# Kernel optimization log

Hardware: AMD Instinct MI355X
Metric: run time of the kernel (lower is better)

Reference implementation:

```python
import jax, jax.numpy as jnp
import numpy as np

N = 4096
IN_F = 256
H = 4
D = 64
WIN = 128
HALF = WIN // 2
TAU = 0.5
TOP_K = 32


def setup_inputs() -> dict:
    key = jax.random.key(0)
    ks = jax.random.split(key, 5)
    node_features = jax.random.normal(ks[0], (N, IN_F), dtype=jnp.float32)
    s = 1.0 / np.sqrt(IN_F)
    Wq = jax.random.normal(ks[1], (IN_F, H * D), dtype=jnp.float32) * s
    bq = jax.random.normal(ks[2], (H * D,), dtype=jnp.float32) * 0.01
    Wk = jax.random.normal(ks[3], (IN_F, H * D), dtype=jnp.float32) * s
    bk = jax.random.normal(ks[4], (H * D,), dtype=jnp.float32) * 0.01
    num_nodes_per_graph = jnp.full((8,), 512, dtype=jnp.int32)  # 8 graphs x 512 = N
    return {"node_features": node_features, "Wq": Wq, "bq": bq, "Wk": Wk,
            "bk": bk, "num_nodes_per_graph": num_nodes_per_graph, "num_relation": 1}


def reference(node_features, Wq, bq, Wk, bk, num_nodes_per_graph, num_relation):
    n = node_features.shape[0]
    scale = jnp.sqrt(jnp.asarray(D, node_features.dtype))

    Q = (node_features @ Wq + bq).reshape(n, H, D)
    K = (node_features @ Wk + bk).reshape(n, H, D)

    # segment boundaries (graph.num_nodes.repeat(num_relation) -> cumsum -> searchsorted)
    segment = jnp.tile(num_nodes_per_graph, num_relation)
    cum = jnp.cumsum(segment)
    i = jnp.arange(n)
    pos = jnp.searchsorted(cum, i, side='right')
    seg_start = jnp.where(pos == 0, 0, cum[jnp.maximum(pos - 1, 0)])
    seg_end = cum[jnp.minimum(pos, cum.shape[0] - 1)]

    start = jnp.maximum(seg_start, i - HALF)  # [N]
    end = jnp.minimum(seg_end, i + HALF)      # [N]

    gather_idx = start[:, None] + jnp.arange(WIN)[None, :]
    valid = gather_idx < end[:, None]
    gi = jnp.clip(gather_idx, 0, n - 1)
    Kw = jnp.where(valid[:, :, None, None], K[gi], 0.0)

    # scores over full window incl. zero padding (faithful: original does not mask softmax)
    scores = jnp.einsum('nhd,nmhd->nhm', Q, Kw) / scale / TAU
    attn = jax.nn.softmax(scores, axis=-1).mean(axis=1)

    # scatter attention rows into dense N x N (padded slots add 0)
    output = jnp.zeros((n, n), node_features.dtype).at[i[:, None], gi].add(
        jnp.where(valid, attn, 0.0))

    # gumbel_softmax_top_k(output, tau, hard=self.k) -> hard=True (k truthy)
    g = jax.random.gumbel(jax.random.key(42), output.shape, output.dtype)
    y_soft = jax.nn.softmax((output + g) / TAU, axis=-1)
    topk_idx = jax.lax.top_k(output, TOP_K)[1]                  # [N, TOP_K]
    y_hard = jnp.zeros_like(output).at[i[:, None], topk_idx].set(1.0)
    y = jax.lax.stop_gradient(y_hard - y_soft) + y_soft
    return y
```

## Files before the change

kernel.cpp:

```cpp
#include <hip/hip_runtime.h>

#define NF   256
#define HD   256
#define NH   4
#define DH   64
#define WINS 128
#define HALFW 64
#define TOPK 32
#define GR   8

__global__ __launch_bounds__(256) void qk_gemm_kernel(
    const float* __restrict__ X,
    const float* __restrict__ Wq, const float* __restrict__ bq,
    const float* __restrict__ Wk, const float* __restrict__ bk,
    float* __restrict__ Qb, float* __restrict__ Kt, int n)
{
    const bool isK = (blockIdx.y != 0);
    const float* W   = isK ? Wk : Wq;
    const float* bia = isK ? bk : bq;

    __shared__ float feat[GR][NF];
    const int rowBase = blockIdx.x * GR;
    const int t = threadIdx.x;

    {
        const float4* src = (const float4*)(X + (size_t)rowBase * NF);
        float4* dst = (float4*)&feat[0][0];
        dst[t]       = src[t];
        dst[t + 256] = src[t + 256];
    }
    __syncthreads();

    float acc[GR];
#pragma unroll
    for (int r = 0; r < GR; ++r) acc[r] = 0.f;

#pragma unroll 4
    for (int k = 0; k < NF; k += 4) {
        float w0 = W[(size_t)(k + 0) * HD + t];
        float w1 = W[(size_t)(k + 1) * HD + t];
        float w2 = W[(size_t)(k + 2) * HD + t];
        float w3 = W[(size_t)(k + 3) * HD + t];
#pragma unroll
        for (int r = 0; r < GR; ++r) {
            float4 f = *(const float4*)&feat[r][k];
            acc[r] += f.x * w0 + f.y * w1 + f.z * w2 + f.w * w3;
        }
    }
    float bias = bia[t];

    if (!isK) {
#pragma unroll
        for (int r = 0; r < GR; ++r)
            Qb[(size_t)(rowBase + r) * HD + t] = acc[r] + bias;
    } else {
        float4* o = (float4*)(Kt + (size_t)t * n + rowBase);
        o[0] = make_float4(acc[0] + bias, acc[1] + bias, acc[2] + bias, acc[3] + bias);
        o[1] = make_float4(acc[4] + bias, acc[5] + bias, acc[6] + bias, acc[7] + bias);
    }
}

__global__ __launch_bounds__(256) void attn_topk_kernel(
    const float* __restrict__ Q,
    const float* __restrict__ KT,
    const int* __restrict__ nnpg, int n_graphs,
    const int* __restrict__ nrel,
    float* __restrict__ out, int n)
{
    const int i    = blockIdx.x;
    const int t    = threadIdx.x;
    const int wave = t >> 6;
    const int lane = t & 63;

    __shared__ float qs[HD];
    __shared__ float pr[NH][WINS];
    __shared__ float attnv[WINS];
    __shared__ float slotval[WINS];

    int R = nrel[0];
    int total = n_graphs * R;
    int seg_start = 0, seg_end = n;
    int cum = 0;
    for (int e = 0; e < total; ++e) {
        int sz = nnpg[e % n_graphs];
        int nc = cum + sz;
        if (i < nc) { seg_start = cum; seg_end = nc; break; }
        cum = nc;
    }
    const int start = max(seg_start, i - HALFW);
    const int end   = min(seg_end,   i + HALFW);
    const int win   = end - start;

    qs[t] = Q[(size_t)i * HD + t];
    __syncthreads();

    const bool v0 = (lane      < win);
    const bool v1 = (lane + 64 < win);
    const int  j0 = v0 ? (start + lane)      : start;
    const int  j1 = v1 ? (start + lane + 64) : start;

    const float* kcol = KT + (size_t)(wave * DH) * n;
    const float* qh   = qs + wave * DH;

    float a0 = 0.f, a1 = 0.f;
#pragma unroll 8
    for (int d = 0; d < DH; ++d) {
        float qd = qh[d];
        const float* col = kcol + (size_t)d * n;
        a0 += qd * col[j0];
        a1 += qd * col[j1];
    }
    a0 = v0 ? a0 * 0.25f : 0.f;
    a1 = v1 ? a1 * 0.25f : 0.f;

    float mx = fmaxf(a0, a1);
#pragma unroll
    for (int off = 32; off > 0; off >>= 1) mx = fmaxf(mx, __shfl_xor(mx, off));
    float e0 = expf(a0 - mx), e1 = expf(a1 - mx);
    float sm = e0 + e1;
#pragma unroll
    for (int off = 32; off > 0; off >>= 1) sm += __shfl_xor(sm, off);
    pr[wave][lane]      = e0 / sm;
    pr[wave][lane + 64] = e1 / sm;
    __syncthreads();

    if (t < WINS) {
        float a = 0.25f * (pr[0][t] + pr[1][t] + pr[2][t] + pr[3][t]);
        attnv[t] = (t < win) ? a : -1.0f;
    }
    __syncthreads();

    if (t < WINS) {
        float v = attnv[t];
        int cnt = 0;
#pragma unroll
        for (int j4 = 0; j4 < WINS / 4; ++j4) {
            float4 a4 = *(const float4*)&attnv[j4 * 4];
            int jb = j4 * 4;
            cnt += (a4.x > v) || (a4.x == v && (jb + 0) < t);
            cnt += (a4.y > v) || (a4.y == v && (jb + 1) < t);
            cnt += (a4.z > v) || (a4.z == v && (jb + 2) < t);
            cnt += (a4.w > v) || (a4.w == v && (jb + 3) < t);
        }
        slotval[t] = (t < win && cnt < TOPK) ? 1.0f : 0.0f;
    }
    __syncthreads();

    float4* orow = (float4*)(out + (size_t)i * n);
    const int n4 = n >> 2;
    for (int c4 = t; c4 < n4; c4 += 256) {
        int c = c4 << 2;
        float4 v4 = make_float4(0.f, 0.f, 0.f, 0.f);
        if (c + 3 >= start && c < end) {
            int o = c - start;
            if (o     >= 0 && o     < WINS) v4.x = slotval[o];
            if (o + 1 >= 0 && o + 1 < WINS) v4.y = slotval[o + 1];
            if (o + 2 >= 0 && o + 2 < WINS) v4.z = slotval[o + 2];
            if (o + 3 >= 0 && o + 3 < WINS) v4.w = slotval[o + 3];
        }
        orow[c4] = v4;
    }
}

extern "C" void kernel_launch(void* const* d_in, const int* in_sizes, int n_in,
                              void* d_out, int out_size, void* d_ws, size_t ws_size,
                              hipStream_t stream)
{
    const float* X  = (const float*)d_in[0];
    const float* Wq = (const float*)d_in[1];
    const float* bq = (const float*)d_in[2];
    const float* Wk = (const float*)d_in[3];
    const float* bk = (const float*)d_in[4];
    const int* nnpg = (const int*)d_in[5];
    const int* nrel = (const int*)d_in[6];

    const int n = in_sizes[0] / NF;
    const int n_graphs = in_sizes[5];

    float* Qb = (float*)d_ws;
    float* Kt = Qb + (size_t)n * HD;
    float* out = (float*)d_out;

    dim3 gg(n / GR, 2);
    qk_gemm_kernel<<<gg, 256, 0, stream>>>(X, Wq, bq, Wk, bk, Qb, Kt, n);
    attn_topk_kernel<<<n, 256, 0, stream>>>(Qb, Kt, nnpg, n_graphs, nrel, out, n);
}
```

Measured before the change: 161.2 us.

## Map one wave per row in attention kernel, split zero fill, drop LDS staging

The attention kernel now gives each wave one output row and loops over the four heads itself. Q values are broadcast with readlane, and top-k ranking happens within the wave, so the block-level syncs and shared Q/probability buffers go away. The dense zero write of the output matrix moves to a separate grid-stride fill kernel, and the attention kernel scatters only the selected ones. The GEMM also stops staging X in LDS and reads it straight from global memory. The costs are an extra kernel launch, the full output written in a separate pass, and one wave now doing four heads of work serially.

```diff
diff --git a/kernel.cpp b/kernel.cpp
--- a/kernel.cpp
+++ b/kernel.cpp
@@ -8,6 +8,11 @@
 #define HALFW 64
 #define TOPK 32
 #define GR   8
+#define NPB  4
+
+__device__ __forceinline__ float readlane_f(float v, int l) {
+    return __uint_as_float(__builtin_amdgcn_readlane(__float_as_uint(v), l));
+}
 
 __global__ __launch_bounds__(256) void qk_gemm_kernel(
     const float* __restrict__ X,
@@ -19,17 +24,9 @@
     const float* W   = isK ? Wk : Wq;
     const float* bia = isK ? bk : bq;
 
-    __shared__ float feat[GR][NF];
+    const int t = threadIdx.x;
     const int rowBase = blockIdx.x * GR;
-    const int t = threadIdx.x;
-
-    {
-        const float4* src = (const float4*)(X + (size_t)rowBase * NF);
-        float4* dst = (float4*)&feat[0][0];
-        dst[t]       = src[t];
-        dst[t + 256] = src[t + 256];
-    }
-    __syncthreads();
+    const float* Xb = X + (size_t)rowBase * NF;
 
     float acc[GR];
 #pragma unroll
@@ -43,7 +40,7 @@
         float w3 = W[(size_t)(k + 3) * HD + t];
 #pragma unroll
         for (int r = 0; r < GR; ++r) {
-            float4 f = *(const float4*)&feat[r][k];
+            float4 f = *(const float4*)(Xb + r * NF + k);
             acc[r] += f.x * w0 + f.y * w1 + f.z * w2 + f.w * w3;
         }
     }
@@ -60,6 +57,14 @@
     }
 }
 
+__global__ __launch_bounds__(256) void fill_zero_kernel(float4* __restrict__ p, int n4)
+{
+    int idx = blockIdx.x * 256 + threadIdx.x;
+    int stride = gridDim.x * 256;
+    float4 z = make_float4(0.f, 0.f, 0.f, 0.f);
+    for (int c = idx; c < n4; c += stride) p[c] = z;
+}
+
 __global__ __launch_bounds__(256) void attn_topk_kernel(
     const float* __restrict__ Q,
     const float* __restrict__ KT,
@@ -67,15 +72,12 @@
     const int* __restrict__ nrel,
     float* __restrict__ out, int n)
 {
-    const int i    = blockIdx.x;
     const int t    = threadIdx.x;
     const int wave = t >> 6;
     const int lane = t & 63;
+    const int i    = blockIdx.x * NPB + wave;
 
-    __shared__ float qs[HD];
-    __shared__ float pr[NH][WINS];
-    __shared__ float attnv[WINS];
-    __shared__ float slotval[WINS];
+    __shared__ float attnv[NPB][WINS];
 
     int R = nrel[0];
     int total = n_graphs * R;
@@ -91,75 +93,69 @@
     const int end   = min(seg_end,   i + HALFW);
     const int win   = end - start;
 
-    qs[t] = Q[(size_t)i * HD + t];
-    __syncthreads();
+    const float* qrow = Q + (size_t)i * HD;
+    float qr[NH];
+#pragma unroll
+    for (int h = 0; h < NH; ++h) qr[h] = qrow[lane + h * DH];
 
     const bool v0 = (lane      < win);
     const bool v1 = (lane + 64 < win);
-    const int  j0 = v0 ? (start + lane)      : start;
-    const int  j1 = v1 ? (start + lane + 64) : start;
+    const int  j0 = start + min(lane,      win - 1);
+    const int  j1 = start + min(lane + 64, win - 1);
 
-    const float* kcol = KT + (size_t)(wave * DH) * n;
-    const float* qh   = qs + wave * DH;
+    float mean0 = 0.f, mean1 = 0.f;
+#pragma unroll
+    for (int h = 0; h < NH; ++h) {
+        const float* base = KT + (size_t)(h * DH) * n;
+        float a0 = 0.f, a1 = 0.f;
+#pragma unroll 8
+        for (int d = 0; d < DH; ++d) {
+            float qd = readlane_f(qr[h], d);
+            const float* col = base + (size_t)d * n;
+            a0 += qd * col[j0];
+            a1 += qd * col[j1];
+        }
+        a0 = v0 ? a0 * 0.25f : 0.f;
+        a1 = v1 ? a1 * 0.25f : 0.f;
 
-    float a0 = 0.f, a1 = 0.f;
-#pragma unroll 8
-    for (int d = 0; d < DH; ++d) {
-        float qd = qh[d];
-        const float* col = kcol + (size_t)d * n;
-        a0 += qd * col[j0];
-        a1 += qd * col[j1];
+        float mx = fmaxf(a0, a1);
+#pragma unroll
+        for (int off = 32; off > 0; off >>= 1) mx = fmaxf(mx, __shfl_xor(mx, off));
+        float e0 = expf(a0 - mx), e1 = expf(a1 - mx);
+        float sm = e0 + e1;
+#pragma unroll
+        for (int off = 32; off > 0; off >>= 1) sm += __shfl_xor(sm, off);
+        float inv = 1.f / sm;
+        mean0 += e0 * inv;
+        mean1 += e1 * inv;
     }
-    a0 = v0 ? a0 * 0.25f : 0.f;
-    a1 = v1 ? a1 * 0.25f : 0.f;
+    mean0 *= 0.25f;
+    mean1 *= 0.25f;
 
-    float mx = fmaxf(a0, a1);
+    attnv[wave][lane]      = v0 ? mean0 : -1.0f;
+    attnv[wave][lane + 64] = v1 ? mean1 : -1.0f;
+
+    float w0v = v0 ? mean0 : -1.0f;
+    float w1v = v1 ? mean1 : -1.0f;
+    int cnt0 = 0, cnt1 = 0;
+    const int s0 = lane, s1 = lane + 64;
 #pragma unroll
-    for (int off = 32; off > 0; off >>= 1) mx = fmaxf(mx, __shfl_xor(mx, off));
-    float e0 = expf(a0 - mx), e1 = expf(a1 - mx);
-    float sm = e0 + e1;
-#pragma unroll
-    for (int off = 32; off > 0; off >>= 1) sm += __shfl_xor(sm, off);
-    pr[wave][lane]      = e0 / sm;
-    pr[wave][lane + 64] = e1 / sm;
-    __syncthreads();
+    for (int j4 = 0; j4 < WINS / 4; ++j4) {
+        float4 a4 = *(const float4*)&attnv[wave][j4 * 4];
+        int jb = j4 * 4;
+        cnt0 += (a4.x > w0v) || (a4.x == w0v && (jb + 0) < s0);
+        cnt0 += (a4.y > w0v) || (a4.y == w0v && (jb + 1) < s0);
+        cnt0 += (a4.z > w0v) || (a4.z == w0v && (jb + 2) < s0);
+        cnt0 += (a4.w > w0v) || (a4.w == w0v && (jb + 3) < s0);
+        cnt1 += (a4.x > w1v) || (a4.x == w1v && (jb + 0) < s1);
+        cnt1 += (a4.y > w1v) || (a4.y == w1v && (jb + 1) < s1);
+        cnt1 += (a4.z > w1v) || (a4.z == w1v && (jb + 2) < s1);
+        cnt1 += (a4.w > w1v) || (a4.w == w1v && (jb + 3) < s1);
+    }
 
-    if (t < WINS) {
-        float a = 0.25f * (pr[0][t] + pr[1][t] + pr[2][t] + pr[3][t]);
-        attnv[t] = (t < win) ? a : -1.0f;
-    }
-    __syncthreads();
-
-    if (t < WINS) {
-        float v = attnv[t];
-        int cnt = 0;
-#pragma unroll
-        for (int j4 = 0; j4 < WINS / 4; ++j4) {
-            float4 a4 = *(const float4*)&attnv[j4 * 4];
-            int jb = j4 * 4;
-            cnt += (a4.x > v) || (a4.x == v && (jb + 0) < t);
-            cnt += (a4.y > v) || (a4.y == v && (jb + 1) < t);
-            cnt += (a4.z > v) || (a4.z == v && (jb + 2) < t);
-            cnt += (a4.w > v) || (a4.w == v && (jb + 3) < t);
-        }
-        slotval[t] = (t < win && cnt < TOPK) ? 1.0f : 0.0f;
-    }
-    __syncthreads();
-
-    float4* orow = (float4*)(out + (size_t)i * n);
-    const int n4 = n >> 2;
-    for (int c4 = t; c4 < n4; c4 += 256) {
-        int c = c4 << 2;
-        float4 v4 = make_float4(0.f, 0.f, 0.f, 0.f);
-        if (c + 3 >= start && c < end) {
-            int o = c - start;
-            if (o     >= 0 && o     < WINS) v4.x = slotval[o];
-            if (o + 1 >= 0 && o + 1 < WINS) v4.y = slotval[o + 1];
-            if (o + 2 >= 0 && o + 2 < WINS) v4.z = slotval[o + 2];
-            if (o + 3 >= 0 && o + 3 < WINS) v4.w = slotval[o + 3];
-        }
-        orow[c4] = v4;
-    }
+    float* orow = out + (size_t)i * n;
+    if (v0 && cnt0 < TOPK) orow[start + s0] = 1.0f;
+    if (v1 && cnt1 < TOPK) orow[start + s1] = 1.0f;
 }
 
 extern "C" void kernel_launch(void* const* d_in, const int* in_sizes, int n_in,
@@ -183,5 +179,8 @@
 
     dim3 gg(n / GR, 2);
     qk_gemm_kernel<<<gg, 256, 0, stream>>>(X, Wq, bq, Wk, bk, Qb, Kt, n);
-    attn_topk_kernel<<<n, 256, 0, stream>>>(Qb, Kt, nnpg, n_graphs, nrel, out, n);
+
+    fill_zero_kernel<<<2048, 256, 0, stream>>>((float4*)out, out_size >> 2);
+
+    attn_topk_kernel<<<n / NPB, NPB * 64, 0, stream>>>(Qb, Kt, nnpg, n_graphs, nrel, out, n);
 }
```

Measured after the change: 172.2 us. 6.8% more time.
